# Kernel optimization log

Measured on AMD Instinct MI355X. Metric: run time of the kernel, lower is better.

Reference implementation:

```python
import jax, jax.numpy as jnp
import numpy as np
import math

T, N, F, A, NH = 2048, 64, 64, 64, 8
QG, QH, DG, DH = 256, 256, 256, 256
HORIZON = 16


def setup_inputs() -> dict:
    key = jax.random.key(0)
    ks = jax.random.split(key, 12)
    s = 0.05  # xavier-ish scale
    return {
        "x_fix": jax.random.normal(ks[0], (T, F), jnp.float32),
        "x_att": jax.random.normal(ks[1], (T, N, A), jnp.float32),
        "train_horizon": HORIZON,
        # query GRUCell: input = fix + 2*A*NH
        "q_gru_w_ih": jax.random.normal(ks[2], (3 * QG, F + 2 * A * NH), jnp.float32) * s,
        "q_gru_w_hh": jax.random.normal(ks[3], (3 * QG, QG), jnp.float32) * s,
        "q_gru_b_ih": jnp.zeros((3 * QG,), jnp.float32),
        "q_gru_b_hh": jnp.zeros((3 * QG,), jnp.float32),
        # q_hidden: input = QG + F + A*NH
        "q_hid_w": jax.random.normal(ks[4], (QH, QG + F + A * NH), jnp.float32) * s,
        "q_hid_b": jnp.zeros((QH,), jnp.float32),
        "weight_q": jax.random.normal(ks[5], (QH, A * NH), jnp.float32) * s,
        # decoder GRU: input = F + A*NH
        "dec_gru_w_ih": jax.random.normal(ks[6], (3 * DG, F + A * NH), jnp.float32) * s,
        "dec_gru_w_hh": jax.random.normal(ks[7], (3 * DG, DG), jnp.float32) * s,
        "dec_gru_b_ih": jnp.zeros((3 * DG,), jnp.float32),
        "dec_gru_b_hh": jnp.zeros((3 * DG,), jnp.float32),
        # dec_hidden: input = DG + F + A*NH + A
        "dec_hid_w": jax.random.normal(ks[8], (DH, DG + F + A * NH + A), jnp.float32) * s,
        "dec_hid_b": jnp.zeros((DH,), jnp.float32),
        "dec_out_w": jax.random.normal(ks[9], (A, DH), jnp.float32) * s,
        "dec_out_b": jnp.zeros((A,), jnp.float32),
    }


def _gru_cell(x, h, w_ih, w_hh, b_ih, b_hh):
    """PyTorch GRUCell math (gate order r,z,n)."""
    gi = w_ih @ x + b_ih
    gh = w_hh @ h + b_hh
    ir, iz, in_ = jnp.split(gi, 3)
    hr, hz, hn = jnp.split(gh, 3)
    r = jax.nn.sigmoid(ir + hr)
    z = jax.nn.sigmoid(iz + hz)
    n = jnp.tanh(in_ + r * hn)
    return (1.0 - z) * n + z * h


def reference(x_fix, x_att, train_horizon,
              q_gru_w_ih, q_gru_w_hh, q_gru_b_ih, q_gru_b_hh,
              q_hid_w, q_hid_b, weight_q,
              dec_gru_w_ih, dec_gru_w_hh, dec_gru_b_ih, dec_gru_b_hh,
              dec_hid_w, dec_hid_b, dec_out_w, dec_out_b):
    t, n_obj, a = x_att.shape
    nh_a = weight_q.shape[1]
    nh = nh_a // a
    scale = 1.0 / math.sqrt(a)

    # ---- recurrent query generation (sequential over time) ----
    def step(carry, inp):
        h, query = carry
        fix_t, att_t = inp                                   # [F], [N, A]
        attw = jax.nn.softmax((query.reshape(nh, a) @ att_t.T) * scale, axis=1)  # [NH, N]
        att_v = (attw @ att_t).reshape(-1)                   # [NH*A]
        h2 = _gru_cell(jnp.concatenate([fix_t, att_v, query]), h,
                       q_gru_w_ih, q_gru_w_hh, q_gru_b_ih, q_gru_b_hh)
        hid = jax.nn.relu(q_hid_w @ jnp.concatenate([h2, fix_t, att_v]) + q_hid_b)
        query2 = hid @ weight_q
        return (h2, query2), (attw, att_v)

    h0 = jnp.zeros((q_gru_w_hh.shape[1],), x_fix.dtype)
    q0 = jnp.ones((nh_a,), x_fix.dtype)
    (q_gru_n, query_n), (attw, att_a) = jax.lax.scan(step, (h0, q0), (x_fix, x_att))

    # ---- decoder (training path; dropout_p=0, noise_std=0 -> identity) ----
    hz = train_horizon
    # replicate-pad attw back hz steps in time, drop last hz: dec_attw[t] = attw[max(t-hz,0)]
    dec_attw = jnp.concatenate(
        [jnp.broadcast_to(attw[:1], (hz,) + attw.shape[1:]), attw[:-hz]], axis=0)  # [T, NH, N]
    dec_att_a = jnp.einsum('thn,tnd->thd', dec_attw, x_att).reshape(t, -1)          # [T, NH*A]
    dec_x = jnp.concatenate([x_fix, dec_att_a], axis=-1)                            # [T, F+NH*A]

    def dec_step(hd, xt):
        hd2 = _gru_cell(xt, hd, dec_gru_w_ih, dec_gru_w_hh, dec_gru_b_ih, dec_gru_b_hh)
        return hd2, hd2

    dg0 = jnp.zeros((dec_gru_w_hh.shape[1],), x_fix.dtype)
    dec_gru_n, dec_gru_a = jax.lax.scan(dec_step, dg0, dec_x)                       # [T, DG]

    feat = jnp.concatenate([dec_gru_a, dec_x], axis=-1)                             # [T, DG+F+NH*A]
    feat_b = jnp.broadcast_to(feat[:, None, :], (t, n_obj, feat.shape[-1]))
    inp = jnp.concatenate([feat_b, x_att], axis=-1)                                 # [T, N, DG+F+NH*A+A]
    hid = jax.nn.relu(inp @ dec_hid_w.T + dec_hid_b)
    pred = jax.nn.relu(hid @ dec_out_w.T + dec_out_b)                               # [T, N, A]

    return pred, attw, q_gru_n, dec_gru_n, query_n
```

## Files before the change

kernel.cpp:

```cpp
#include <hip/hip_runtime.h>
#include <math.h>

#define TT 2048
#define HZ 16
#define NBLK 32
#define NTH 512

#define OUT_ATTW   (2048*64*64)
#define OUT_QGRU   (OUT_ATTW + 2048*8*64)
#define OUT_DECGRU (OUT_QGRU + 256)
#define OUT_QN     (OUT_DECGRU + 256)

#define WSO_MB1    0
#define WSO_QACC   8192
#define WSO_QCNT   14336
#define WSO_ZEND   14464
#define WSO_GIFIX  14464
#define WSO_HIDFIX (WSO_GIFIX + 2048*768*4)
#define WSO_W2T    (WSO_HIDFIX + 2048*256*4)
#define WSO_DAVA   (WSO_W2T + 256*64*4)
#define WSO_DECH   (WSO_DAVA + 2048*512*4)
#define WSO_FEAT   (WSO_DECH + 2048*256*4)
#define WSO_SBUF   (WSO_FEAT + 2048*832*4)

__device__ __forceinline__ float warp_sum(float v) {
#pragma unroll
  for (int o = 32; o > 0; o >>= 1) v += __shfl_down(v, o, 64);
  return v;
}
__device__ __forceinline__ float warp_max(float v) {
#pragma unroll
  for (int o = 32; o > 0; o >>= 1) v = fmaxf(v, __shfl_down(v, o, 64));
  return v;
}
__device__ __forceinline__ float sigf(float x) { return 1.f / (1.f + __expf(-x)); }
__device__ __forceinline__ float dot4(float4 a, float4 b) {
  return a.x*b.x + a.y*b.y + a.z*b.z + a.w*b.w;
}
__device__ __forceinline__ unsigned long long aload64(const unsigned long long* p) {
  return __hip_atomic_load(p, __ATOMIC_RELAXED, __HIP_MEMORY_SCOPE_AGENT);
}
__device__ __forceinline__ void astore64(unsigned long long* p, unsigned long long v) {
  __hip_atomic_store(p, v, __ATOMIC_RELAXED, __HIP_MEMORY_SCOPE_AGENT);
}
__device__ __forceinline__ unsigned long long mbpack(float f, unsigned tag) {
  return ((unsigned long long)tag << 32) | (unsigned long long)__float_as_uint(f);
}
__device__ __forceinline__ float mbpoll(const unsigned long long* p, unsigned tag) {
  unsigned long long v = aload64(p);
  while ((unsigned)(v >> 32) != tag) {
    __builtin_amdgcn_s_sleep(1);
    v = aload64(p);
  }
  return __uint_as_float((unsigned)v);
}

__global__ void transpose_k(const float* __restrict__ w2,
                            float* __restrict__ w2T) {
  int e = blockIdx.x * 256 + threadIdx.x;
  int r = e >> 6, a = e & 63;
  w2T[e] = w2[a * 256 + r];
}

__global__ void __launch_bounds__(256) gemm64(
    const float* __restrict__ X, int ldx,
    const float* __restrict__ W, int ldw, int woff,
    const float* __restrict__ bias,
    float* __restrict__ C, int crows, int K) {
  __shared__ float Xs[64 * 65];
  __shared__ float Ws[64 * 65];
  int t0 = blockIdx.x * 64, r0 = blockIdx.y * 64;
  int tid = threadIdx.x;
  int u = tid & 15, v = tid >> 4;
  float acc[4][4];
#pragma unroll
  for (int i = 0; i < 4; i++)
#pragma unroll
    for (int j = 0; j < 4; j++) acc[i][j] = 0.f;

  for (int kc = 0; kc < K; kc += 64) {
    for (int idx = tid; idx < 4096; idx += 256) {
      int row = idx >> 6, col = idx & 63;
      Xs[row * 65 + col] = X[(size_t)(t0 + row) * ldx + kc + col];
      Ws[row * 65 + col] = W[(size_t)(r0 + row) * ldw + woff + kc + col];
    }
    __syncthreads();
#pragma unroll 8
    for (int k = 0; k < 64; k++) {
      float xs[4], ws[4];
#pragma unroll
      for (int i = 0; i < 4; i++) xs[i] = Xs[(v + 16 * i) * 65 + k];
#pragma unroll
      for (int j = 0; j < 4; j++) ws[j] = Ws[(u + 16 * j) * 65 + k];
#pragma unroll
      for (int i = 0; i < 4; i++)
#pragma unroll
        for (int j = 0; j < 4; j++) acc[i][j] += xs[i] * ws[j];
    }
    __syncthreads();
  }
#pragma unroll
  for (int i = 0; i < 4; i++)
#pragma unroll
    for (int j = 0; j < 4; j++) {
      int t = t0 + v + 16 * i, r = r0 + u + 16 * j;
      C[(size_t)t * crows + r] = acc[i][j] + bias[r];
    }
}

__global__ void __launch_bounds__(512) seq_kernel(
    const float* __restrict__ x_fix,
    const float* __restrict__ x_att,
    const float* __restrict__ w_ih,
    const float* __restrict__ w_hh,
    const float* __restrict__ b_hh,
    const float* __restrict__ q_hid_w,
    const float* __restrict__ wq,
    const float* __restrict__ dwih,
    const float* __restrict__ dwhh,
    const float* __restrict__ dbih,
    const float* __restrict__ dbhh,
    const float* __restrict__ gi_fix,
    const float* __restrict__ hid_fix,
    unsigned long long* __restrict__ mb1,
    float* __restrict__ qacc,
    unsigned* __restrict__ qcnt,
    float* __restrict__ dava,
    float* __restrict__ dec_hist,
    float* __restrict__ out) {
  __shared__ float att_s[64 * 65];
  __shared__ float ring_s[16][512];
  __shared__ __align__(16) float avq_s[1024];
  __shared__ float qk_s[512];
  __shared__ __align__(16) float xcat_s[576];
  __shared__ __align__(16) float hid8_s[8];
  __shared__ __align__(16) float h_s[256];
  __shared__ __align__(16) float dech_s[256];
  __shared__ float g_s[4][8];
  __shared__ float dg_s[4][8];

  const int tid = threadIdx.x;
  const int bid = blockIdx.x;
  const int lane = tid & 63, wv = tid >> 6;

  for (int i = tid; i < 1024; i += NTH) avq_s[i] = (i >= 512) ? 1.f : 0.f;
  if (tid < 256) { h_s[tid] = 0.f; dech_s[tid] = 0.f; }
  {
    const float4* g4 = (const float4*)x_att;
    float4 a = g4[tid * 2], b = g4[tid * 2 + 1];
    int row = tid >> 3, c0 = (tid & 7) * 8;
    float* d = &att_s[row * 65 + c0];
    d[0]=a.x; d[1]=a.y; d[2]=a.z; d[3]=a.w; d[4]=b.x; d[5]=b.y; d[6]=b.z; d[7]=b.w;
  }
  if (tid < 64) xcat_s[tid] = x_fix[tid];
  __syncthreads();

  for (int t = 0; t <= TT; ++t) {
    if (t > 0) {
      {
        float f = mbpoll(mb1 + (size_t)((t - 1) & 1) * 512 + tid, (unsigned)t);
        int b = tid >> 4, j = tid & 15;
        if (j < 8) h_s[b * 8 + j] = f;
        else dech_s[b * 8 + j - 8] = f;
        if (t >= 2 && tid < 16)
          __hip_atomic_store(&qacc[(size_t)((t - 1) % 3) * 512 + bid * 16 + tid],
                             0.f, __ATOMIC_RELAXED, __HIP_MEMORY_SCOPE_AGENT);
      }
      __syncthreads();
      {
        int row = bid * 8 + wv;
        const float4* W = (const float4*)(q_hid_w + (size_t)row * 832);
        float acc = dot4(W[lane], ((const float4*)h_s)[lane]);
        acc += dot4(W[80 + lane], ((const float4*)avq_s)[lane]);
        acc += dot4(W[144 + lane], ((const float4*)avq_s)[64 + lane]);
        float s = warp_sum(acc);
        if (lane == 0)
          hid8_s[wv] = fmaxf(s + hid_fix[(size_t)(t - 1) * 256 + row], 0.f);
      }
      __syncthreads();
      {
        float hv[8];
#pragma unroll
        for (int r = 0; r < 8; r++) hv[r] = hid8_s[r];
        float partial = 0.f;
#pragma unroll
        for (int r = 0; r < 8; r++)
          partial += hv[r] * wq[(size_t)(bid * 8 + r) * 512 + tid];
        __hip_atomic_fetch_add(&qacc[(size_t)(t % 3) * 512 + tid], partial,
                               __ATOMIC_RELAXED, __HIP_MEMORY_SCOPE_AGENT);
        asm volatile("s_waitcnt vmcnt(0)" ::: "memory");
      }
      __syncthreads();
      if (tid == 0) {
        __hip_atomic_fetch_add(qcnt, 1u, __ATOMIC_RELAXED,
                               __HIP_MEMORY_SCOPE_AGENT);
        unsigned target = 32u * (unsigned)t;
        while (__hip_atomic_load(qcnt, __ATOMIC_RELAXED,
                                 __HIP_MEMORY_SCOPE_AGENT) < target)
          __builtin_amdgcn_s_sleep(1);
      }
      __syncthreads();
      {
        float qv = __hip_atomic_load(&qacc[(size_t)(t % 3) * 512 + tid],
                                     __ATOMIC_RELAXED, __HIP_MEMORY_SCOPE_AGENT);
        avq_s[512 + tid] = qv;
        if (t == TT) {
          if (bid == 0) {
            if (tid < 256) {
              out[OUT_QGRU + tid] = h_s[tid];
              out[OUT_DECGRU + tid] = dech_s[tid];
            }
            out[OUT_QN + tid] = qv;
          }
          break;
        }
      }
      __syncthreads();
    }

    float4 pfa, pfb;
    {
      int tn = (t + 1 < TT) ? t + 1 : t;
      const float4* g4 = (const float4*)(x_att + (size_t)tn * 4096);
      pfa = g4[tid * 2];
      pfb = g4[tid * 2 + 1];
    }
    {
      float acc = 0.f;
#pragma unroll 16
      for (int a = 0; a < 64; a++)
        acc += avq_s[512 + wv * 64 + a] * att_s[lane * 65 + a];
      acc *= 0.125f;
      float m = __shfl(warp_max(acc), 0, 64);
      float e = __expf(acc - m);
      float s = __shfl(warp_sum(e), 0, 64);
      qk_s[wv * 64 + lane] = e / s;
    }
    {
      const float* rg = (t == 0) ? &qk_s[0] : ring_s[(t >= 16) ? (t & 15) : 0];
      float av = 0.f, dv = 0.f;
#pragma unroll 8
      for (int n = 0; n < 64; n++) {
        float xv = att_s[n * 65 + lane];
        av += qk_s[wv * 64 + n] * xv;
        dv += rg[wv * 64 + n] * xv;
      }
      avq_s[wv * 64 + lane] = av;
      xcat_s[64 + wv * 64 + lane] = dv;
    }
    __syncthreads();
    {
      float accg[3], acch[3];
      int rows[3];
#pragma unroll
      for (int k = 0; k < 3; k++) {
        int m = wv * 3 + k;
        rows[k] = ((m >> 3) * 256) + bid * 8 + (m & 7);
        accg[k] = 0.f; acch[k] = 0.f;
      }
      const float4* in4 = (const float4*)avq_s;
#pragma unroll
      for (int c0 = 0; c0 < 4; c0++) {
        int c = lane + 64 * c0;
        float4 v = in4[c];
#pragma unroll
        for (int k = 0; k < 3; k++) {
          const float4* W = (const float4*)(w_ih + (size_t)rows[k] * 1088 + 64);
          accg[k] += dot4(W[c], v);
        }
      }
      {
        const float4* h4 = (const float4*)h_s;
        float4 vh = h4[lane];
#pragma unroll
        for (int k = 0; k < 3; k++) {
          const float4* Wh = (const float4*)(w_hh + (size_t)rows[k] * 256);
          acch[k] += dot4(Wh[lane], vh);
        }
      }
#pragma unroll
      for (int k = 0; k < 3; k++) {
        int m = wv * 3 + k;
        int gate = m >> 3, idx = m & 7;
        if (gate < 2) {
          float s = warp_sum(accg[k] + acch[k]);
          if (lane == 0)
            g_s[gate][idx] = s + gi_fix[(size_t)t * 768 + rows[k]] + b_hh[rows[k]];
        } else {
          float sg = warp_sum(accg[k]);
          float sh = warp_sum(acch[k]);
          if (lane == 0) {
            g_s[2][idx] = sg + gi_fix[(size_t)t * 768 + rows[k]];
            g_s[3][idx] = sh + b_hh[rows[k]];
          }
        }
      }
    }
    {
      float accg[3], acch[3];
      int rows[3];
#pragma unroll
      for (int k = 0; k < 3; k++) {
        int m = wv * 3 + k;
        rows[k] = ((m >> 3) * 256) + bid * 8 + (m & 7);
        accg[k] = 0.f; acch[k] = 0.f;
      }
      const float4* x4 = (const float4*)xcat_s;
#pragma unroll
      for (int c0 = 0; c0 < 3; c0++) {
        int c = lane + 64 * c0;
        if (c < 144) {
          float4 v = x4[c];
#pragma unroll
          for (int k = 0; k < 3; k++) {
            const float4* W = (const float4*)(dwih + (size_t)rows[k] * 576);
            accg[k] += dot4(W[c], v);
          }
        }
      }
      {
        const float4* dh4 = (const float4*)dech_s;
        float4 vh = dh4[lane];
#pragma unroll
        for (int k = 0; k < 3; k++) {
          const float4* Wh = (const float4*)(dwhh + (size_t)rows[k] * 256);
          acch[k] += dot4(Wh[lane], vh);
        }
      }
#pragma unroll
      for (int k = 0; k < 3; k++) {
        int m = wv * 3 + k;
        int gate = m >> 3, idx = m & 7;
        if (gate < 2) {
          float s = warp_sum(accg[k] + acch[k]);
          if (lane == 0)
            dg_s[gate][idx] = s + dbih[rows[k]] + dbhh[rows[k]];
        } else {
          float sg = warp_sum(accg[k]);
          float sh = warp_sum(acch[k]);
          if (lane == 0) {
            dg_s[2][idx] = sg + dbih[rows[k]];
            dg_s[3][idx] = sh + dbhh[rows[k]];
          }
        }
      }
    }
    __syncthreads();
    if (tid < 8) {
      float r = sigf(g_s[0][tid]), z = sigf(g_s[1][tid]);
      float nn = tanhf(g_s[2][tid] + r * g_s[3][tid]);
      float h2 = (1.f - z) * nn + z * h_s[bid * 8 + tid];
      astore64(&mb1[(size_t)(t & 1) * 512 + bid * 16 + tid],
               mbpack(h2, (unsigned)(t + 1)));
    } else if (tid < 16) {
      int i = tid - 8;
      float r = sigf(dg_s[0][i]), z = sigf(dg_s[1][i]);
      float nn = tanhf(dg_s[2][i] + r * dg_s[3][i]);
      float d2 = (1.f - z) * nn + z * dech_s[bid * 8 + i];
      astore64(&mb1[(size_t)(t & 1) * 512 + bid * 16 + tid],
               mbpack(d2, (unsigned)(t + 1)));
      dec_hist[(size_t)t * 256 + bid * 8 + i] = d2;
    }
    if (tid < 16) {
      out[OUT_ATTW + (size_t)t * 512 + bid * 16 + tid] = qk_s[bid * 16 + tid];
      dava[(size_t)t * 512 + bid * 16 + tid] = xcat_s[64 + bid * 16 + tid];
    }
    ring_s[t & 15][tid] = qk_s[tid];
    {
      int row = tid >> 3, c0 = (tid & 7) * 8;
      float* d = &att_s[row * 65 + c0];
      d[0]=pfa.x; d[1]=pfa.y; d[2]=pfa.z; d[3]=pfa.w;
      d[4]=pfb.x; d[5]=pfb.y; d[6]=pfb.z; d[7]=pfb.w;
    }
    if (tid >= 448) {
      int i = tid - 448;
      int tn = (t + 1 < TT) ? t + 1 : t;
      xcat_s[i] = x_fix[tn * 64 + i];
    }
  }
}

__global__ void featcopy(const float* __restrict__ dec_hist,
                         const float* __restrict__ x_fix,
                         const float* __restrict__ dava,
                         float* __restrict__ feat) {
  int t = blockIdx.x, tid = threadIdx.x;
  float* f = feat + (size_t)t * 832;
  f[tid] = dec_hist[(size_t)t * 256 + tid];
  if (tid < 64) f[256 + tid] = x_fix[t * 64 + tid];
  for (int i = tid; i < 512; i += 256) f[320 + i] = dava[(size_t)t * 512 + i];
}

__global__ void __launch_bounds__(256) final_k(
    const float* __restrict__ x_att,
    const float* __restrict__ s,
    const float* __restrict__ w1,
    const float* __restrict__ w2T,
    const float* __restrict__ b2,
    float* __restrict__ pred) {
  __shared__ float att_s[4096];
  __shared__ float s_s[256];
  __shared__ float hid_s[32 * 256];
  int t = blockIdx.x, tid = threadIdx.x, lane = tid & 63, wv = tid >> 6;
  for (int i = tid; i < 4096; i += 256) att_s[i] = x_att[(size_t)t * 4096 + i];
  s_s[tid] = s[(size_t)t * 256 + tid];
  float4 w1v[16];
  const float4* W1a4 = (const float4*)(w1 + (size_t)tid * 896 + 832);
#pragma unroll
  for (int q = 0; q < 16; q++) w1v[q] = W1a4[q];
  float bb = b2[lane];
  __syncthreads();
  for (int ch = 0; ch < 2; ch++) {
    for (int nl = 0; nl < 32; nl++) {
      int n = ch * 32 + nl;
      const float4* a4 = (const float4*)(att_s + n * 64);
      float acc = s_s[tid];
#pragma unroll
      for (int q = 0; q < 16; q++) acc += dot4(w1v[q], a4[q]);
      hid_s[nl * 256 + tid] = fmaxf(acc, 0.f);
    }
    __syncthreads();
    float accb[8];
#pragma unroll
    for (int j = 0; j < 8; j++) accb[j] = bb;
    for (int r = 0; r < 256; r++) {
      float w = w2T[r * 64 + lane];
#pragma unroll
      for (int j = 0; j < 8; j++) accb[j] += w * hid_s[(wv * 8 + j) * 256 + r];
    }
#pragma unroll
    for (int j = 0; j < 8; j++) {
      int n = ch * 32 + wv * 8 + j;
      pred[(size_t)t * 4096 + n * 64 + lane] = fmaxf(accb[j], 0.f);
    }
    __syncthreads();
  }
}

extern "C" void kernel_launch(void* const* d_in, const int* in_sizes, int n_in,
                              void* d_out, int out_size, void* d_ws, size_t ws_size,
                              hipStream_t stream) {
  const float* x_fix = (const float*)d_in[0];
  const float* x_att = (const float*)d_in[1];
  const float* qwih = (const float*)d_in[3];
  const float* qwhh = (const float*)d_in[4];
  const float* qbih = (const float*)d_in[5];
  const float* qbhh = (const float*)d_in[6];
  const float* qhw = (const float*)d_in[7];
  const float* qhb = (const float*)d_in[8];
  const float* wq = (const float*)d_in[9];
  const float* dwih = (const float*)d_in[10];
  const float* dwhh = (const float*)d_in[11];
  const float* dbih = (const float*)d_in[12];
  const float* dbhh = (const float*)d_in[13];
  const float* w1 = (const float*)d_in[14];
  const float* b1 = (const float*)d_in[15];
  const float* w2 = (const float*)d_in[16];
  const float* b2 = (const float*)d_in[17];
  float* out = (float*)d_out;

  char* ws = (char*)d_ws;
  unsigned long long* mb1 = (unsigned long long*)(ws + WSO_MB1);
  float* qacc = (float*)(ws + WSO_QACC);
  unsigned* qcnt = (unsigned*)(ws + WSO_QCNT);
  float* gi_fix = (float*)(ws + WSO_GIFIX);
  float* hid_fix = (float*)(ws + WSO_HIDFIX);
  float* w2T = (float*)(ws + WSO_W2T);
  float* dava = (float*)(ws + WSO_DAVA);
  float* dec_hist = (float*)(ws + WSO_DECH);
  float* feat = (float*)(ws + WSO_FEAT);
  float* sbuf = (float*)(ws + WSO_SBUF);

  hipMemsetAsync(ws, 0, WSO_ZEND, stream);

  transpose_k<<<64, 256, 0, stream>>>(w2, w2T);
  gemm64<<<dim3(32, 12), 256, 0, stream>>>(x_fix, 64, qwih, 1088, 0, qbih,
                                           gi_fix, 768, 64);
  gemm64<<<dim3(32, 4), 256, 0, stream>>>(x_fix, 64, qhw, 832, 256, qhb,
                                          hid_fix, 256, 64);

  seq_kernel<<<NBLK, NTH, 0, stream>>>(x_fix, x_att, qwih, qwhh, qbhh,
                                       qhw, wq, dwih, dwhh, dbih, dbhh,
                                       gi_fix, hid_fix, mb1, qacc, qcnt,
                                       dava, dec_hist, out);

  featcopy<<<2048, 256, 0, stream>>>(dec_hist, x_fix, dava, feat);
  gemm64<<<dim3(32, 4), 256, 0, stream>>>(feat, 832, w1, 896, 0, b1,
                                          sbuf, 256, 832);
  final_k<<<2048, 256, 0, stream>>>(x_att, sbuf, w1, w2T, b2, out);
}
```

Baseline: 22.66 ms.

## Replace atomic-add query reduction and counter barrier with tagged per-block mailboxes

The query-projection step now runs on only 8 of the 32 blocks. Each of those blocks computes 32 rows of q_hidden, with its q_hid_w and weight_q slices kept in registers for the whole run. Each block publishes its partial query vector as a step-tagged 64-bit value, and every block polls all 8 mailboxes and sums them itself. This replaces the float atomic-add accumulation, the buffer zeroing and the global counter barrier, cutting an atomic round trip and a barrier per timestep. The cost is a large register footprint, more work on fewer blocks, and 8 polled loads per thread; the partial sums also end up in a fixed summation order.

```diff
diff --git a/kernel.cpp b/kernel.cpp
--- a/kernel.cpp
+++ b/kernel.cpp
@@ -12,9 +12,7 @@
 #define OUT_QN     (OUT_DECGRU + 256)
 
 #define WSO_MB1    0
-#define WSO_QACC   8192
-#define WSO_QCNT   14336
-#define WSO_ZEND   14464
+#define WSO_ZEND   8192
 #define WSO_GIFIX  14464
 #define WSO_HIDFIX (WSO_GIFIX + 2048*768*4)
 #define WSO_W2T    (WSO_HIDFIX + 2048*256*4)
@@ -22,6 +20,7 @@
 #define WSO_DECH   (WSO_DAVA + 2048*512*4)
 #define WSO_FEAT   (WSO_DECH + 2048*256*4)
 #define WSO_SBUF   (WSO_FEAT + 2048*832*4)
+#define WSO_QPART  WSO_SBUF
 
 __device__ __forceinline__ float warp_sum(float v) {
 #pragma unroll
@@ -123,8 +122,7 @@
     const float* __restrict__ gi_fix,
     const float* __restrict__ hid_fix,
     unsigned long long* __restrict__ mb1,
-    float* __restrict__ qacc,
-    unsigned* __restrict__ qcnt,
+    unsigned long long* __restrict__ qpart,
     float* __restrict__ dava,
     float* __restrict__ dec_hist,
     float* __restrict__ out) {
@@ -133,7 +131,7 @@
   __shared__ __align__(16) float avq_s[1024];
   __shared__ float qk_s[512];
   __shared__ __align__(16) float xcat_s[576];
-  __shared__ __align__(16) float hid8_s[8];
+  __shared__ float hid32_s[32];
   __shared__ __align__(16) float h_s[256];
   __shared__ __align__(16) float dech_s[256];
   __shared__ float g_s[4][8];
@@ -142,6 +140,21 @@
   const int tid = threadIdx.x;
   const int bid = blockIdx.x;
   const int lane = tid & 63, wv = tid >> 6;
+  const int wbid = bid & 7;
+
+  float4 wB[4][3];
+#pragma unroll
+  for (int k = 0; k < 4; k++) {
+    const float4* W =
+        (const float4*)(q_hid_w + (size_t)(wbid * 32 + wv * 4 + k) * 832);
+    wB[k][0] = W[lane];
+    wB[k][1] = W[80 + lane];
+    wB[k][2] = W[144 + lane];
+  }
+  float wC[32];
+#pragma unroll
+  for (int r = 0; r < 32; r++)
+    wC[r] = wq[(size_t)(wbid * 32 + r) * 512 + tid];
 
   for (int i = tid; i < 1024; i += NTH) avq_s[i] = (i >= 512) ? 1.f : 0.f;
   if (tid < 256) { h_s[tid] = 0.f; dech_s[tid] = 0.f; }
@@ -162,47 +175,44 @@
         int b = tid >> 4, j = tid & 15;
         if (j < 8) h_s[b * 8 + j] = f;
         else dech_s[b * 8 + j - 8] = f;
-        if (t >= 2 && tid < 16)
-          __hip_atomic_store(&qacc[(size_t)((t - 1) % 3) * 512 + bid * 16 + tid],
-                             0.f, __ATOMIC_RELAXED, __HIP_MEMORY_SCOPE_AGENT);
       }
       __syncthreads();
+      if (bid < 8) {
+        const float4* h4 = (const float4*)h_s;
+        const float4* a4 = (const float4*)avq_s;
+        float4 vh = h4[lane], v1 = a4[lane], v2 = a4[64 + lane];
+#pragma unroll
+        for (int k = 0; k < 4; k++) {
+          float acc = dot4(wB[k][0], vh) + dot4(wB[k][1], v1) + dot4(wB[k][2], v2);
+          float s = warp_sum(acc);
+          if (lane == 0)
+            hid32_s[wv * 4 + k] = fmaxf(
+                s + hid_fix[(size_t)(t - 1) * 256 + wbid * 32 + wv * 4 + k], 0.f);
+        }
+      }
+      __syncthreads();
+      if (bid < 8) {
+        float part = 0.f;
+#pragma unroll
+        for (int r = 0; r < 32; r++) part += hid32_s[r] * wC[r];
+        astore64(&qpart[(size_t)wbid * 512 + tid], mbpack(part, (unsigned)t));
+      }
       {
-        int row = bid * 8 + wv;
-        const float4* W = (const float4*)(q_hid_w + (size_t)row * 832);
-        float acc = dot4(W[lane], ((const float4*)h_s)[lane]);
-        acc += dot4(W[80 + lane], ((const float4*)avq_s)[lane]);
-        acc += dot4(W[144 + lane], ((const float4*)avq_s)[64 + lane]);
-        float s = warp_sum(acc);
-        if (lane == 0)
-          hid8_s[wv] = fmaxf(s + hid_fix[(size_t)(t - 1) * 256 + row], 0.f);
-      }
-      __syncthreads();
-      {
-        float hv[8];
-#pragma unroll
-        for (int r = 0; r < 8; r++) hv[r] = hid8_s[r];
-        float partial = 0.f;
-#pragma unroll
-        for (int r = 0; r < 8; r++)
-          partial += hv[r] * wq[(size_t)(bid * 8 + r) * 512 + tid];
-        __hip_atomic_fetch_add(&qacc[(size_t)(t % 3) * 512 + tid], partial,
-                               __ATOMIC_RELAXED, __HIP_MEMORY_SCOPE_AGENT);
-        asm volatile("s_waitcnt vmcnt(0)" ::: "memory");
-      }
-      __syncthreads();
-      if (tid == 0) {
-        __hip_atomic_fetch_add(qcnt, 1u, __ATOMIC_RELAXED,
-                               __HIP_MEMORY_SCOPE_AGENT);
-        unsigned target = 32u * (unsigned)t;
-        while (__hip_atomic_load(qcnt, __ATOMIC_RELAXED,
-                                 __HIP_MEMORY_SCOPE_AGENT) < target)
+        unsigned long long v[8];
+        for (;;) {
+#pragma unroll
+          for (int w = 0; w < 8; w++)
+            v[w] = aload64(&qpart[(size_t)w * 512 + tid]);
+          bool ok = true;
+#pragma unroll
+          for (int w = 0; w < 8; w++)
+            ok = ok && ((unsigned)(v[w] >> 32) == (unsigned)t);
+          if (ok) break;
           __builtin_amdgcn_s_sleep(1);
-      }
-      __syncthreads();
-      {
-        float qv = __hip_atomic_load(&qacc[(size_t)(t % 3) * 512 + tid],
-                                     __ATOMIC_RELAXED, __HIP_MEMORY_SCOPE_AGENT);
+        }
+        float qv = 0.f;
+#pragma unroll
+        for (int w = 0; w < 8; w++) qv += __uint_as_float((unsigned)v[w]);
         avq_s[512 + tid] = qv;
         if (t == TT) {
           if (bid == 0) {
@@ -461,8 +471,7 @@
 
   char* ws = (char*)d_ws;
   unsigned long long* mb1 = (unsigned long long*)(ws + WSO_MB1);
-  float* qacc = (float*)(ws + WSO_QACC);
-  unsigned* qcnt = (unsigned*)(ws + WSO_QCNT);
+  unsigned long long* qpart = (unsigned long long*)(ws + WSO_QPART);
   float* gi_fix = (float*)(ws + WSO_GIFIX);
   float* hid_fix = (float*)(ws + WSO_HIDFIX);
   float* w2T = (float*)(ws + WSO_W2T);
@@ -472,6 +481,7 @@
   float* sbuf = (float*)(ws + WSO_SBUF);
 
   hipMemsetAsync(ws, 0, WSO_ZEND, stream);
+  hipMemsetAsync(ws + WSO_QPART, 0, 8 * 512 * 8, stream);
 
   transpose_k<<<64, 256, 0, stream>>>(w2, w2T);
   gemm64<<<dim3(32, 12), 256, 0, stream>>>(x_fix, 64, qwih, 1088, 0, qbih,
@@ -481,7 +491,7 @@
 
   seq_kernel<<<NBLK, NTH, 0, stream>>>(x_fix, x_att, qwih, qwhh, qbhh,
                                        qhw, wq, dwih, dwhh, dbih, dbhh,
-                                       gi_fix, hid_fix, mb1, qacc, qcnt,
+                                       gi_fix, hid_fix, mb1, qpart,
                                        dava, dec_hist, out);
 
   featcopy<<<2048, 256, 0, stream>>>(dec_hist, x_fix, dava, feat);
```

Result: slower. 32.91 ms (+45.2%).

## Overlap decoder GRU step with query barrier wait and keep weights in registers

Applied to the files above, without the earlier changes.

Moves the decoder GRU gate computation for step t into the window between posting the query-count atomic and spinning on the grid barrier, so that decoder work hides the cross-block synchronisation latency. Also preloads this block's query GRU input/hidden weight slices, q_hidden row, weight_q column and biases into registers once, instead of reloading them from global memory every timestep. This raises register pressure, which could reduce occupancy or cause spills, and it changes the ordering of the mailbox writes for decoder state.

```diff
diff --git a/kernel.cpp b/kernel.cpp
--- a/kernel.cpp
+++ b/kernel.cpp
@@ -143,6 +143,77 @@
   const int bid = blockIdx.x;
   const int lane = tid & 63, wv = tid >> 6;
 
+  int rowsQ[3];
+#pragma unroll
+  for (int k = 0; k < 3; k++) {
+    int m = wv * 3 + k;
+    rowsQ[k] = ((m >> 3) * 256) + bid * 8 + (m & 7);
+  }
+
+  float4 wGi[3][4];
+  float4 wGh[3];
+  float bhh_r[3], dbi_r[3], dbh_r[3];
+#pragma unroll
+  for (int k = 0; k < 3; k++) {
+    const float4* Wi = (const float4*)(w_ih + (size_t)rowsQ[k] * 1088 + 64);
+#pragma unroll
+    for (int c0 = 0; c0 < 4; c0++) wGi[k][c0] = Wi[lane + 64 * c0];
+    wGh[k] = ((const float4*)(w_hh + (size_t)rowsQ[k] * 256))[lane];
+    bhh_r[k] = b_hh[rowsQ[k]];
+    dbi_r[k] = dbih[rowsQ[k]];
+    dbh_r[k] = dbhh[rowsQ[k]];
+  }
+  float4 wBq[3];
+  {
+    const float4* W = (const float4*)(q_hid_w + (size_t)(bid * 8 + wv) * 832);
+    wBq[0] = W[lane];
+    wBq[1] = W[80 + lane];
+    wBq[2] = W[144 + lane];
+  }
+  float wqr[8];
+#pragma unroll
+  for (int r = 0; r < 8; r++) wqr[r] = wq[(size_t)(bid * 8 + r) * 512 + tid];
+
+  auto dec_gates = [&]() {
+    float accg[3], acch[3];
+#pragma unroll
+    for (int k = 0; k < 3; k++) { accg[k] = 0.f; acch[k] = 0.f; }
+    const float4* x4 = (const float4*)xcat_s;
+#pragma unroll
+    for (int c0 = 0; c0 < 3; c0++) {
+      int c = lane + 64 * c0;
+      if (c < 144) {
+        float4 v = x4[c];
+#pragma unroll
+        for (int k = 0; k < 3; k++) {
+          const float4* W = (const float4*)(dwih + (size_t)rowsQ[k] * 576);
+          accg[k] += dot4(W[c], v);
+        }
+      }
+    }
+    {
+      float4 vh = ((const float4*)dech_s)[lane];
+#pragma unroll
+      for (int k = 0; k < 3; k++) {
+        const float4* Wh = (const float4*)(dwhh + (size_t)rowsQ[k] * 256);
+        acch[k] += dot4(Wh[lane], vh);
+      }
+    }
+#pragma unroll
+    for (int k = 0; k < 3; k++) {
+      int m = wv * 3 + k;
+      int gate = m >> 3, idx = m & 7;
+      if (gate < 2) {
+        float s = warp_sum(accg[k] + acch[k]);
+        if (lane == 0) dg_s[gate][idx] = s + dbi_r[k] + dbh_r[k];
+      } else {
+        float sg = warp_sum(accg[k]);
+        float sh = warp_sum(acch[k]);
+        if (lane == 0) { dg_s[2][idx] = sg + dbi_r[k]; dg_s[3][idx] = sh + dbh_r[k]; }
+      }
+    }
+  };
+
   for (int i = tid; i < 1024; i += NTH) avq_s[i] = (i >= 512) ? 1.f : 0.f;
   if (tid < 256) { h_s[tid] = 0.f; dech_s[tid] = 0.f; }
   {
@@ -168,14 +239,13 @@
       }
       __syncthreads();
       {
-        int row = bid * 8 + wv;
-        const float4* W = (const float4*)(q_hid_w + (size_t)row * 832);
-        float acc = dot4(W[lane], ((const float4*)h_s)[lane]);
-        acc += dot4(W[80 + lane], ((const float4*)avq_s)[lane]);
-        acc += dot4(W[144 + lane], ((const float4*)avq_s)[64 + lane]);
+        float hfx = hid_fix[(size_t)(t - 1) * 256 + bid * 8 + wv];
+        const float4* h4 = (const float4*)h_s;
+        const float4* a4 = (const float4*)avq_s;
+        float acc = dot4(wBq[0], h4[lane]) + dot4(wBq[1], a4[lane]) +
+                    dot4(wBq[2], a4[64 + lane]);
         float s = warp_sum(acc);
-        if (lane == 0)
-          hid8_s[wv] = fmaxf(s + hid_fix[(size_t)(t - 1) * 256 + row], 0.f);
+        if (lane == 0) hid8_s[wv] = fmaxf(s + hfx, 0.f);
       }
       __syncthreads();
       {
@@ -184,16 +254,39 @@
         for (int r = 0; r < 8; r++) hv[r] = hid8_s[r];
         float partial = 0.f;
 #pragma unroll
-        for (int r = 0; r < 8; r++)
-          partial += hv[r] * wq[(size_t)(bid * 8 + r) * 512 + tid];
+        for (int r = 0; r < 8; r++) partial += hv[r] * wqr[r];
         __hip_atomic_fetch_add(&qacc[(size_t)(t % 3) * 512 + tid], partial,
                                __ATOMIC_RELAXED, __HIP_MEMORY_SCOPE_AGENT);
         asm volatile("s_waitcnt vmcnt(0)" ::: "memory");
       }
       __syncthreads();
-      if (tid == 0) {
+      if (tid == 0)
         __hip_atomic_fetch_add(qcnt, 1u, __ATOMIC_RELAXED,
                                __HIP_MEMORY_SCOPE_AGENT);
+      if (t < TT) {
+        {
+          const float* rg = ring_s[(t >= 16) ? (t & 15) : 0];
+          float dv = 0.f;
+#pragma unroll 8
+          for (int n = 0; n < 64; n++) dv += rg[wv * 64 + n] * att_s[n * 65 + lane];
+          xcat_s[64 + wv * 64 + lane] = dv;
+        }
+        __syncthreads();
+        dec_gates();
+        __syncthreads();
+        if (tid < 8) {
+          float r = sigf(dg_s[0][tid]), z = sigf(dg_s[1][tid]);
+          float nn = tanhf(dg_s[2][tid] + r * dg_s[3][tid]);
+          float d2 = (1.f - z) * nn + z * dech_s[bid * 8 + tid];
+          astore64(&mb1[(size_t)(t & 1) * 512 + bid * 16 + 8 + tid],
+                   mbpack(d2, (unsigned)(t + 1)));
+          dec_hist[(size_t)t * 256 + bid * 8 + tid] = d2;
+        } else if (tid >= 16 && tid < 32) {
+          int k2 = tid - 16;
+          dava[(size_t)t * 512 + bid * 16 + k2] = xcat_s[64 + bid * 16 + k2];
+        }
+      }
+      if (tid == 0) {
         unsigned target = 32u * (unsigned)t;
         while (__hip_atomic_load(qcnt, __ATOMIC_RELAXED,
                                  __HIP_MEMORY_SCOPE_AGENT) < target)
@@ -225,6 +318,9 @@
       pfa = g4[tid * 2];
       pfb = g4[tid * 2 + 1];
     }
+    float gfx[3];
+#pragma unroll
+    for (int k = 0; k < 3; k++) gfx[k] = gi_fix[(size_t)t * 768 + rowsQ[k]];
     {
       float acc = 0.f;
 #pragma unroll 16
@@ -237,46 +333,35 @@
       qk_s[wv * 64 + lane] = e / s;
     }
     {
-      const float* rg = (t == 0) ? &qk_s[0] : ring_s[(t >= 16) ? (t & 15) : 0];
-      float av = 0.f, dv = 0.f;
+      float av = 0.f;
 #pragma unroll 8
-      for (int n = 0; n < 64; n++) {
-        float xv = att_s[n * 65 + lane];
-        av += qk_s[wv * 64 + n] * xv;
-        dv += rg[wv * 64 + n] * xv;
-      }
+      for (int n = 0; n < 64; n++)
+        av += qk_s[wv * 64 + n] * att_s[n * 65 + lane];
       avq_s[wv * 64 + lane] = av;
+    }
+    if (t == 0) {
+      float dv = 0.f;
+#pragma unroll 8
+      for (int n = 0; n < 64; n++)
+        dv += qk_s[wv * 64 + n] * att_s[n * 65 + lane];
       xcat_s[64 + wv * 64 + lane] = dv;
     }
     __syncthreads();
     {
       float accg[3], acch[3];
-      int rows[3];
-#pragma unroll
-      for (int k = 0; k < 3; k++) {
-        int m = wv * 3 + k;
-        rows[k] = ((m >> 3) * 256) + bid * 8 + (m & 7);
-        accg[k] = 0.f; acch[k] = 0.f;
-      }
+#pragma unroll
+      for (int k = 0; k < 3; k++) { accg[k] = 0.f; acch[k] = 0.f; }
       const float4* in4 = (const float4*)avq_s;
 #pragma unroll
       for (int c0 = 0; c0 < 4; c0++) {
-        int c = lane + 64 * c0;
-        float4 v = in4[c];
-#pragma unroll
-        for (int k = 0; k < 3; k++) {
-          const float4* W = (const float4*)(w_ih + (size_t)rows[k] * 1088 + 64);
-          accg[k] += dot4(W[c], v);
-        }
+        float4 v = in4[lane + 64 * c0];
+#pragma unroll
+        for (int k = 0; k < 3; k++) accg[k] += dot4(wGi[k][c0], v);
       }
       {
-        const float4* h4 = (const float4*)h_s;
-        float4 vh = h4[lane];
-#pragma unroll
-        for (int k = 0; k < 3; k++) {
-          const float4* Wh = (const float4*)(w_hh + (size_t)rows[k] * 256);
-          acch[k] += dot4(Wh[lane], vh);
-        }
+        float4 vh = ((const float4*)h_s)[lane];
+#pragma unroll
+        for (int k = 0; k < 3; k++) acch[k] += dot4(wGh[k], vh);
       }
 #pragma unroll
       for (int k = 0; k < 3; k++) {
@@ -284,67 +369,15 @@
         int gate = m >> 3, idx = m & 7;
         if (gate < 2) {
           float s = warp_sum(accg[k] + acch[k]);
-          if (lane == 0)
-            g_s[gate][idx] = s + gi_fix[(size_t)t * 768 + rows[k]] + b_hh[rows[k]];
+          if (lane == 0) g_s[gate][idx] = s + gfx[k] + bhh_r[k];
         } else {
           float sg = warp_sum(accg[k]);
           float sh = warp_sum(acch[k]);
-          if (lane == 0) {
-            g_s[2][idx] = sg + gi_fix[(size_t)t * 768 + rows[k]];
-            g_s[3][idx] = sh + b_hh[rows[k]];
-          }
+          if (lane == 0) { g_s[2][idx] = sg + gfx[k]; g_s[3][idx] = sh + bhh_r[k]; }
         }
       }
     }
-    {
-      float accg[3], acch[3];
-      int rows[3];
-#pragma unroll
-      for (int k = 0; k < 3; k++) {
-        int m = wv * 3 + k;
-        rows[k] = ((m >> 3) * 256) + bid * 8 + (m & 7);
-        accg[k] = 0.f; acch[k] = 0.f;
-      }
-      const float4* x4 = (const float4*)xcat_s;
-#pragma unroll
-      for (int c0 = 0; c0 < 3; c0++) {
-        int c = lane + 64 * c0;
-        if (c < 144) {
-          float4 v = x4[c];
-#pragma unroll
-          for (int k = 0; k < 3; k++) {
-            const float4* W = (const float4*)(dwih + (size_t)rows[k] * 576);
-            accg[k] += dot4(W[c], v);
-          }
-        }
-      }
-      {
-        const float4* dh4 = (const float4*)dech_s;
-        float4 vh = dh4[lane];
-#pragma unroll
-        for (int k = 0; k < 3; k++) {
-          const float4* Wh = (const float4*)(dwhh + (size_t)rows[k] * 256);
-          acch[k] += dot4(Wh[lane], vh);
-        }
-      }
-#pragma unroll
-      for (int k = 0; k < 3; k++) {
-        int m = wv * 3 + k;
-        int gate = m >> 3, idx = m & 7;
-        if (gate < 2) {
-          float s = warp_sum(accg[k] + acch[k]);
-          if (lane == 0)
-            dg_s[gate][idx] = s + dbih[rows[k]] + dbhh[rows[k]];
-        } else {
-          float sg = warp_sum(accg[k]);
-          float sh = warp_sum(acch[k]);
-          if (lane == 0) {
-            dg_s[2][idx] = sg + dbih[rows[k]];
-            dg_s[3][idx] = sh + dbhh[rows[k]];
-          }
-        }
-      }
-    }
+    if (t == 0) dec_gates();
     __syncthreads();
     if (tid < 8) {
       float r = sigf(g_s[0][tid]), z = sigf(g_s[1][tid]);
@@ -352,7 +385,7 @@
       float h2 = (1.f - z) * nn + z * h_s[bid * 8 + tid];
       astore64(&mb1[(size_t)(t & 1) * 512 + bid * 16 + tid],
                mbpack(h2, (unsigned)(t + 1)));
-    } else if (tid < 16) {
+    } else if (t == 0 && tid < 16) {
       int i = tid - 8;
       float r = sigf(dg_s[0][i]), z = sigf(dg_s[1][i]);
       float nn = tanhf(dg_s[2][i] + r * dg_s[3][i]);
@@ -363,7 +396,8 @@
     }
     if (tid < 16) {
       out[OUT_ATTW + (size_t)t * 512 + bid * 16 + tid] = qk_s[bid * 16 + tid];
-      dava[(size_t)t * 512 + bid * 16 + tid] = xcat_s[64 + bid * 16 + tid];
+      if (t == 0)
+        dava[(size_t)t * 512 + bid * 16 + tid] = xcat_s[64 + bid * 16 + tid];
     }
     ring_s[t & 15][tid] = qk_s[tid];
     {
```

Result: faster. 18.35 ms (-19.0%).
